# Optimization experiments

Hardware: AMD Instinct MI355X
Metric: run time of the kernel (lower is better)

Reference implementation:

```python
import jax, jax.numpy as jnp
import numpy as np

N = 8192
SQUARE_SIZE = 10.0
NEIGHBOURHOOD = 1.0
THRESHOLD = 1.0
DECAY = 0.9


def setup_inputs() -> dict:
    key = jax.random.key(0)
    k1, k2, k3, k4 = jax.random.split(key, 4)
    # Random 2D topology on a square, as in SpikingLayer.__init__
    topo = jax.random.uniform(k1, (N, 2), dtype=jnp.float32) * SQUARE_SIZE
    # Pairwise squared distances without the [N,N,2] intermediate
    sq = jnp.sum(topo * topo, axis=1)  # [N]
    d2 = sq[:, None] + sq[None, :] - 2.0 * (topo @ topo.T)  # [N,N]
    mask = (d2 <= NEIGHBOURHOOD * NEIGHBOURHOOD).astype(jnp.float32)
    # Per-node weight rows, zeroed outside the neighbourhood radius
    W = jax.random.normal(k2, (N, N), dtype=jnp.float32) * mask
    # Random initial firing state (0/1) so dynamics are non-trivial
    f0 = (jax.random.uniform(k3, (N,)) > 0.5).astype(jnp.float32)
    v0 = jnp.zeros((N,), dtype=jnp.float32)
    x = jax.random.normal(k4, (N,), dtype=jnp.float32)  # unused, as in torch forward
    return {"W": W, "f0": f0, "v0": v0, "x": x, "num_steps": 64}


def reference(W, f0, v0, x, num_steps):
    # One scan step == one call to SpikingLayer.forward():
    #   node_x = W @ is_firing  (fused over all nodes)
    #   LIF update: v = decay*v + node_x; spike if v >= threshold; reset on spike
    def step(carry, _):
        v, f = carry
        u = W @ f                      # [N] weighted input from firing neighbours
        v = DECAY * v + u
        spike = v >= THRESHOLD         # bool [N]
        f_new = spike.astype(v.dtype)
        v = jnp.where(spike, 0.0, v)   # reset fired neurons
        return (v, f_new), f_new

    (_, _), firing_matrix = jax.lax.scan(step, (v0, f0), None, length=num_steps)
    return firing_matrix  # [num_steps, N], the accumulated firing_matrix
```

## Files before the change

kernel.cpp:

```cpp
#include <hip/hip_runtime.h>

#define NN 8192
#define STEPS 64
#define DECAYF 0.9f
#define THRESHF 1.0f
#define K_MAX 384
#define K_SEG 192
#define KITER 24
#define LROWS 32
#define LPITCH 385

#define CBLOCKS 256
#define STHREADS 576
#define MBSTRIDE 16

typedef unsigned long long u64;
typedef unsigned int u32;

__device__ __forceinline__ void pub_store(u64* p, u64 v) {
    __hip_atomic_store(p, v, __ATOMIC_RELAXED, __HIP_MEMORY_SCOPE_AGENT);
}
__device__ __forceinline__ u64 pub_load(const u64* p) {
    return __hip_atomic_load(p, __ATOMIC_RELAXED, __HIP_MEMORY_SCOPE_AGENT);
}

__global__ __launch_bounds__(STHREADS) void spiking_fused(
        const float* __restrict__ W,
        const float* __restrict__ f0,
        const float* __restrict__ v0,
        float* __restrict__ out,
        u64* __restrict__ fdata) {
    __shared__ u64 lds_ell[LROWS * LPITCH];
    __shared__ u32 lds_fbits[2][CBLOCKS];
    __shared__ u32 lds_spike[8];
    __shared__ int lds_cnt[STEPS];
    __shared__ int lds_flag;

    const int tid  = threadIdx.x;
    const int wave = tid >> 6;
    const int lane = tid & 63;
    const int bid  = blockIdx.x;

    if (tid < STEPS) lds_cnt[tid] = 0;
    if (tid == 0) lds_flag = 0;

    if (wave == 0) {
        float f = (lane < 32) ? f0[bid * 32 + lane] : 0.0f;
        u64 m = __ballot(f != 0.0f);
        if (lane == 0)
            pub_store(&fdata[(size_t)bid * MBSTRIDE],
                      (1ull << 32) | (u32)(m & 0xffffffffull));
    }

    {
        const u64 lmask = (1ull << lane) - 1ull;
        for (int hr = wave; hr < 2 * LROWS; hr += 9) {
            const int rloc = hr >> 1;
            const int half = hr & 1;
            const int cbase = half * (NN / 2);
            const float4* wr4 = (const float4*)
                (W + (size_t)(bid * LROWS + rloc) * NN + cbase);
            u64* pr = lds_ell + rloc * LPITCH + half * K_SEG;

            float4 wv[16];
            #pragma unroll
            for (int i = 0; i < 16; ++i)
                wv[i] = wr4[lane + 64 * i];

            int base = 0;
            #pragma unroll
            for (int i = 0; i < 16; ++i) {
                const int col0 = cbase + (lane + 64 * i) * 4;
                #pragma unroll
                for (int comp = 0; comp < 4; ++comp) {
                    float val = (comp == 0) ? wv[i].x : (comp == 1) ? wv[i].y
                              : (comp == 2) ? wv[i].z : wv[i].w;
                    u64 m = __ballot(val != 0.0f);
                    if (val != 0.0f) {
                        int idx = base + __popcll(m & lmask);
                        if (idx < K_SEG)
                            pr[idx] = ((u64)(u32)(col0 + comp) << 32)
                                    | (u64)__float_as_uint(val);
                    }
                    base += __popcll(m);
                }
            }
            const int cap = (base < K_SEG) ? base : K_SEG;
            for (int j = cap + lane; j < K_SEG; j += 64) pr[j] = 0ull;
        }
    }
    __syncthreads();

    if (wave == 0) {
        for (int s = 0; s < STEPS; ++s) {
            const u64* slot = fdata + (size_t)(s & 1) * CBLOCKS * MBSTRIDE;
            const u32 want = (u32)(s + 1);
            u32* fb = lds_fbits[s & 1];
            u32 pend = 0xFu;
            for (;;) {
                #pragma unroll
                for (int k = 0; k < 4; ++k) {
                    if ((pend >> k) & 1u) {
                        u64 w = pub_load(&slot[(size_t)(lane + 64 * k) * MBSTRIDE]);
                        if ((u32)(w >> 32) == want) {
                            fb[lane + 64 * k] = (u32)w;
                            pend &= ~(1u << k);
                        }
                    }
                }
                if (__all(pend == 0)) break;
                __builtin_amdgcn_s_sleep(2);
            }
            if (lane == 0)
                __hip_atomic_store(&lds_flag, s + 1, __ATOMIC_RELEASE,
                                   __HIP_MEMORY_SCOPE_WORKGROUP);
        }
    } else {
        const int g    = wave - 1;
        const int rloc = g * 4 + (lane >> 4);
        const int row  = bid * LROWS + rloc;
        const int l16  = lane & 15;

        u32 ecol[KITER]; float eval[KITER];
        const u64* pr = lds_ell + rloc * LPITCH;
        #pragma unroll
        for (int k = 0; k < KITER; ++k) {
            u64 p = pr[l16 + 16 * k];
            ecol[k] = (u32)(p >> 32);
            eval[k] = __uint_as_float((u32)p);
        }
        float vreg = v0[row];

        for (int s = 0; s < STEPS; ++s) {
            while (__hip_atomic_load(&lds_flag, __ATOMIC_ACQUIRE,
                                     __HIP_MEMORY_SCOPE_WORKGROUP) < s + 1) {}
            const u32* fb = lds_fbits[s & 1];

            double a0 = 0.0, a1 = 0.0, a2 = 0.0;
            #pragma unroll
            for (int k = 0; k < KITER; k += 3) {
                u32 c0 = ecol[k],     w0 = fb[c0 >> 5];
                u32 c1 = ecol[k + 1], w1 = fb[c1 >> 5];
                u32 c2 = ecol[k + 2], w2 = fb[c2 >> 5];
                a0 += (double)(((w0 >> (c0 & 31)) & 1u) ? eval[k]     : 0.0f);
                a1 += (double)(((w1 >> (c1 & 31)) & 1u) ? eval[k + 1] : 0.0f);
                a2 += (double)(((w2 >> (c2 & 31)) & 1u) ? eval[k + 2] : 0.0f);
            }
            double acc = (a0 + a1) + a2;
            #pragma unroll
            for (int m = 8; m >= 1; m >>= 1)
                acc += __shfl_xor(acc, m, 64);

            float u  = (float)acc;
            float vv = __fadd_rn(__fmul_rn(DECAYF, vreg), u);
            int fire = (vv >= THRESHF);
            vreg = fire ? 0.0f : vv;

            u64 bal = __ballot(fire);
            int old = -1;
            if (lane == 0) {
                u32 bits4 = ((u32)(bal       ) & 1u)
                          | (((u32)(bal >> 16) & 1u) << 1)
                          | (((u32)(bal >> 32) & 1u) << 2)
                          | (((u32)(bal >> 48) & 1u) << 3);
                __hip_atomic_store(&lds_spike[g], bits4, __ATOMIC_RELAXED,
                                   __HIP_MEMORY_SCOPE_WORKGROUP);
                old = __hip_atomic_fetch_add(&lds_cnt[s], 1, __ATOMIC_ACQ_REL,
                                             __HIP_MEMORY_SCOPE_WORKGROUP);
            }
            old = __shfl(old, 0, 64);
            if (old == 7) {
                u32 b = (lane < 8) ? ((lds_spike[lane] & 0xFu) << (4 * lane)) : 0u;
                b |= __shfl_xor(b, 1, 64);
                b |= __shfl_xor(b, 2, 64);
                b |= __shfl_xor(b, 4, 64);
                if (lane == 0)
                    pub_store(&fdata[((size_t)((s + 1) & 1) * CBLOCKS + bid) * MBSTRIDE],
                              ((u64)(u32)(s + 2) << 32) | b);
            }

            if (l16 == 0)
                out[(size_t)s * NN + row] = fire ? 1.0f : 0.0f;
        }
    }
}

extern "C" void kernel_launch(void* const* d_in, const int* in_sizes, int n_in,
                              void* d_out, int out_size, void* d_ws, size_t ws_size,
                              hipStream_t stream) {
    const float* W  = (const float*)d_in[0];
    const float* f0 = (const float*)d_in[1];
    const float* v0 = (const float*)d_in[2];
    float* out = (float*)d_out;

    u64* fdata = (u64*)d_ws;

    spiking_fused<<<dim3(CBLOCKS), dim3(STHREADS), 0, stream>>>(
        W, f0, v0, out, fdata);
}
```

Baseline: 558.7 us.

## Stream W rows through a per-wave LDS ring via async global-to-LDS loads

The ELL compaction prologue used to load a whole half-row of W (16 float4 per lane) into registers and then scan it. It now streams each half-row in 256-float chunks through a 4-entry per-wave LDS ring using global_load_lds, keeping three chunks in flight while the current one is compacted. The goal is to overlap the dominant 256 MB read of W with the ballot/popcount compaction work and to cut register pressure. The cost is an extra 9x4 KB of LDS per block and hand-written vmcnt waits whose correctness depends on exact in-flight counts. Wave-to-row assignment is also rotated.

```diff
diff --git a/kernel.cpp b/kernel.cpp
--- a/kernel.cpp
+++ b/kernel.cpp
@@ -14,6 +14,10 @@
 #define STHREADS 576
 #define MBSTRIDE 16
 
+#define CHUNKF 256
+#define RINGC 4
+#define AHEAD 3
+
 typedef unsigned long long u64;
 typedef unsigned int u32;
 
@@ -22,6 +26,11 @@
 }
 __device__ __forceinline__ u64 pub_load(const u64* p) {
     return __hip_atomic_load(p, __ATOMIC_RELAXED, __HIP_MEMORY_SCOPE_AGENT);
+}
+__device__ __forceinline__ void dma16(const float* g, float* l) {
+    __builtin_amdgcn_global_load_lds(
+        (const __attribute__((address_space(1))) float*)g,
+        (__attribute__((address_space(3))) float*)l, 16, 0, 0);
 }
 
 __global__ __launch_bounds__(STHREADS) void spiking_fused(
@@ -31,6 +40,7 @@
         float* __restrict__ out,
         u64* __restrict__ fdata) {
     __shared__ u64 lds_ell[LROWS * LPITCH];
+    __shared__ float lds_stage[9 * RINGC * CHUNKF];
     __shared__ u32 lds_fbits[2][CBLOCKS];
     __shared__ u32 lds_spike[8];
     __shared__ int lds_cnt[STEPS];
@@ -54,39 +64,56 @@
 
     {
         const u64 lmask = (1ull << lane) - 1ull;
-        for (int hr = wave; hr < 2 * LROWS; hr += 9) {
-            const int rloc = hr >> 1;
-            const int half = hr & 1;
-            const int cbase = half * (NN / 2);
-            const float4* wr4 = (const float4*)
-                (W + (size_t)(bid * LROWS + rloc) * NN + cbase);
-            u64* pr = lds_ell + rloc * LPITCH + half * K_SEG;
-
-            float4 wv[16];
+        const int start = (wave + 1) % 9;
+        const int nhr   = (2 * LROWS - 1 - start) / 9 + 1;
+        const int tch   = nhr * 16;
+        float* ring = lds_stage + wave * (RINGC * CHUNKF);
+
+        auto issue = [&](int t) {
+            const int hr = start + 9 * (t >> 4);
+            const int c  = t & 15;
+            const float* src = W + (size_t)(bid * LROWS + (hr >> 1)) * NN
+                             + (hr & 1) * (NN / 2) + c * CHUNKF + lane * 4;
+            dma16(src, ring + (t & (RINGC - 1)) * CHUNKF);
+        };
+
+        issue(0); issue(1); issue(2);
+        int base = 0;
+        for (int t = 0; t < tch; ++t) {
+            const int hr = t * 0 + start + 9 * (t >> 4);
+            const int c  = t & 15;
+            u64* pr = lds_ell + (hr >> 1) * LPITCH + (hr & 1) * K_SEG;
+            if (c == 0) base = 0;
+
+            if (t + AHEAD < tch)
+                asm volatile("s_waitcnt vmcnt(2)" ::: "memory");
+            else
+                asm volatile("s_waitcnt vmcnt(0)" ::: "memory");
+
+            float4 w4 = *(const float4*)
+                (ring + (t & (RINGC - 1)) * CHUNKF + lane * 4);
+
+            const int col0 = (hr & 1) * (NN / 2) + c * CHUNKF + lane * 4;
             #pragma unroll
-            for (int i = 0; i < 16; ++i)
-                wv[i] = wr4[lane + 64 * i];
-
-            int base = 0;
-            #pragma unroll
-            for (int i = 0; i < 16; ++i) {
-                const int col0 = cbase + (lane + 64 * i) * 4;
-                #pragma unroll
-                for (int comp = 0; comp < 4; ++comp) {
-                    float val = (comp == 0) ? wv[i].x : (comp == 1) ? wv[i].y
-                              : (comp == 2) ? wv[i].z : wv[i].w;
-                    u64 m = __ballot(val != 0.0f);
-                    if (val != 0.0f) {
-                        int idx = base + __popcll(m & lmask);
-                        if (idx < K_SEG)
-                            pr[idx] = ((u64)(u32)(col0 + comp) << 32)
-                                    | (u64)__float_as_uint(val);
-                    }
-                    base += __popcll(m);
+            for (int comp = 0; comp < 4; ++comp) {
+                float val = (comp == 0) ? w4.x : (comp == 1) ? w4.y
+                          : (comp == 2) ? w4.z : w4.w;
+                u64 m = __ballot(val != 0.0f);
+                if (val != 0.0f) {
+                    int idx = base + __popcll(m & lmask);
+                    if (idx < K_SEG)
+                        pr[idx] = ((u64)(u32)(col0 + comp) << 32)
+                                | (u64)__float_as_uint(val);
                 }
-            }
-            const int cap = (base < K_SEG) ? base : K_SEG;
-            for (int j = cap + lane; j < K_SEG; j += 64) pr[j] = 0ull;
+                base += __popcll(m);
+            }
+
+            if (t + AHEAD < tch) issue(t + AHEAD);
+
+            if (c == 15) {
+                const int cap = (base < K_SEG) ? base : K_SEG;
+                for (int j = cap + lane; j < K_SEG; j += 64) pr[j] = 0ull;
+            }
         }
     }
     __syncthreads();
```

Result: slower. 579.9 us (+3.8%).

## Stream W rows into LDS via async DMA ring during ELL compaction

Applied to the files above, without the earlier changes.

The W-to-ELL compaction moves from all nine waves into the eight compute waves, so each wave now builds ELL only for its own four rows. Each wave streams 1 KB chunks of W through a four-buffer LDS ring using global_load_lds, so the next chunks load while the current one is compacted. The aim is to overlap global loads with the ballot and popcount compaction instead of holding 16 float4 per lane in registers. Only three chunks are in flight per wave, fewer outstanding loads than before, and correctness relies on the compiler inserting waits for the async LDS DMA.

```diff
diff --git a/kernel.cpp b/kernel.cpp
--- a/kernel.cpp
+++ b/kernel.cpp
@@ -14,6 +14,8 @@
 #define STHREADS 576
 #define MBSTRIDE 16
 
+#define CHUNKF 256
+
 typedef unsigned long long u64;
 typedef unsigned int u32;
 
@@ -22,6 +24,11 @@
 }
 __device__ __forceinline__ u64 pub_load(const u64* p) {
     return __hip_atomic_load(p, __ATOMIC_RELAXED, __HIP_MEMORY_SCOPE_AGENT);
+}
+__device__ __forceinline__ void dma16(const float* g, float* l) {
+    __builtin_amdgcn_global_load_lds(
+        (const __attribute__((address_space(1))) float*)g,
+        (__attribute__((address_space(3))) float*)l, 16, 0, 0);
 }
 
 __global__ __launch_bounds__(STHREADS) void spiking_fused(
@@ -31,6 +38,10 @@
         float* __restrict__ out,
         u64* __restrict__ fdata) {
     __shared__ u64 lds_ell[LROWS * LPITCH];
+    __shared__ __align__(16) float bufA[8 * CHUNKF];
+    __shared__ __align__(16) float bufB[8 * CHUNKF];
+    __shared__ __align__(16) float bufC[8 * CHUNKF];
+    __shared__ __align__(16) float bufD[8 * CHUNKF];
     __shared__ u32 lds_fbits[2][CBLOCKS];
     __shared__ u32 lds_spike[8];
     __shared__ int lds_cnt[STEPS];
@@ -50,44 +61,6 @@
         if (lane == 0)
             pub_store(&fdata[(size_t)bid * MBSTRIDE],
                       (1ull << 32) | (u32)(m & 0xffffffffull));
-    }
-
-    {
-        const u64 lmask = (1ull << lane) - 1ull;
-        for (int hr = wave; hr < 2 * LROWS; hr += 9) {
-            const int rloc = hr >> 1;
-            const int half = hr & 1;
-            const int cbase = half * (NN / 2);
-            const float4* wr4 = (const float4*)
-                (W + (size_t)(bid * LROWS + rloc) * NN + cbase);
-            u64* pr = lds_ell + rloc * LPITCH + half * K_SEG;
-
-            float4 wv[16];
-            #pragma unroll
-            for (int i = 0; i < 16; ++i)
-                wv[i] = wr4[lane + 64 * i];
-
-            int base = 0;
-            #pragma unroll
-            for (int i = 0; i < 16; ++i) {
-                const int col0 = cbase + (lane + 64 * i) * 4;
-                #pragma unroll
-                for (int comp = 0; comp < 4; ++comp) {
-                    float val = (comp == 0) ? wv[i].x : (comp == 1) ? wv[i].y
-                              : (comp == 2) ? wv[i].z : wv[i].w;
-                    u64 m = __ballot(val != 0.0f);
-                    if (val != 0.0f) {
-                        int idx = base + __popcll(m & lmask);
-                        if (idx < K_SEG)
-                            pr[idx] = ((u64)(u32)(col0 + comp) << 32)
-                                    | (u64)__float_as_uint(val);
-                    }
-                    base += __popcll(m);
-                }
-            }
-            const int cap = (base < K_SEG) ? base : K_SEG;
-            for (int j = cap + lane; j < K_SEG; j += 64) pr[j] = 0ull;
-        }
     }
     __syncthreads();
 
@@ -116,8 +89,64 @@
                                    __HIP_MEMORY_SCOPE_WORKGROUP);
         }
     } else {
-        const int g    = wave - 1;
-        const int rloc = g * 4 + (lane >> 4);
+        const int gx   = wave - 1;
+        const int rl0  = gx << 2;
+
+        {
+            const u64 lmask = (1ull << lane) - 1ull;
+            float* const myA = bufA + gx * CHUNKF;
+            float* const myB = bufB + gx * CHUNKF;
+            float* const myC = bufC + gx * CHUNKF;
+            float* const myD = bufD + gx * CHUNKF;
+
+            auto issue = [&](int t, float* obj) {
+                if (t < 128) {
+                    const int hrl = t >> 4, c = t & 15;
+                    const int row = rl0 + (hrl >> 1);
+                    const float* src = W
+                        + (size_t)(bid * LROWS + row) * NN
+                        + (hrl & 1) * (NN / 2) + c * CHUNKF + lane * 4;
+                    dma16(src, obj + lane * 4);
+                }
+            };
+            int base = 0;
+            auto compact = [&](int t, const float* obj) {
+                const int hrl = t >> 4, c = t & 15;
+                const int rloc = rl0 + (hrl >> 1);
+                const int half = hrl & 1;
+                u64* pr = lds_ell + rloc * LPITCH + half * K_SEG;
+                if (c == 0) base = 0;
+                float4 w4 = *(const float4*)(obj + lane * 4);
+                const int col0 = half * (NN / 2) + c * CHUNKF + lane * 4;
+                #pragma unroll
+                for (int comp = 0; comp < 4; ++comp) {
+                    float val = (comp == 0) ? w4.x : (comp == 1) ? w4.y
+                              : (comp == 2) ? w4.z : w4.w;
+                    u64 m = __ballot(val != 0.0f);
+                    if (val != 0.0f) {
+                        int idx = base + __popcll(m & lmask);
+                        if (idx < K_SEG)
+                            pr[idx] = ((u64)(u32)(col0 + comp) << 32)
+                                    | (u64)__float_as_uint(val);
+                    }
+                    base += __popcll(m);
+                }
+                if (c == 15) {
+                    const int cap = (base < K_SEG) ? base : K_SEG;
+                    for (int j = cap + lane; j < K_SEG; j += 64) pr[j] = 0ull;
+                }
+            };
+
+            issue(0, myA); issue(1, myB); issue(2, myC);
+            for (int t = 0; t < 128; t += 4) {
+                issue(t + 3, myD); compact(t,     myA);
+                issue(t + 4, myA); compact(t + 1, myB);
+                issue(t + 5, myB); compact(t + 2, myC);
+                issue(t + 6, myC); compact(t + 3, myD);
+            }
+        }
+
+        const int rloc = rl0 + (lane >> 4);
         const int row  = bid * LROWS + rloc;
         const int l16  = lane & 15;
 
@@ -163,7 +192,7 @@
                           | (((u32)(bal >> 16) & 1u) << 1)
                           | (((u32)(bal >> 32) & 1u) << 2)
                           | (((u32)(bal >> 48) & 1u) << 3);
-                __hip_atomic_store(&lds_spike[g], bits4, __ATOMIC_RELAXED,
+                __hip_atomic_store(&lds_spike[gx], bits4, __ATOMIC_RELAXED,
                                    __HIP_MEMORY_SCOPE_WORKGROUP);
                 old = __hip_atomic_fetch_add(&lds_cnt[s], 1, __ATOMIC_ACQ_REL,
                                              __HIP_MEMORY_SCOPE_WORKGROUP);
```

New measurement: 566.1 us. No clear change (+1.3%).
